# Performance work log

Hardware: AMD Instinct MI355X
Metric: run time of the kernel (lower is better)

## Reference

```python
import jax, jax.numpy as jnp
import numpy as np
import math

NLAT, NLON, LMAX, MMAX = 128, 256, 50, 50
K = 3  # three_nn

# ---- precompute: Clenshaw-Curtis quadrature (torch_harmonics 'equiangular') ----
def _cc_nodes_weights(n):
    Nn = n - 1
    theta = np.pi * np.arange(n) / Nn
    v = np.zeros(n)
    for k in range(1, Nn // 2 + 1):
        b = 1.0 if 2 * k == Nn else 2.0
        v += b * np.cos(2 * k * theta) / (4 * k * k - 1)
    w = (2.0 / Nn) * (1.0 - v)
    w[0] *= 0.5
    w[-1] *= 0.5
    return np.cos(theta), w

# ---- precompute: orthonormal associated Legendre P_l^m(cos theta), csphase ----
def _legpoly(lmax, mmax, cost):
    sint = np.sqrt(np.clip(1.0 - cost ** 2, 0.0, None))
    p = np.zeros((mmax, lmax, cost.shape[0]))
    pmm = np.full(cost.shape[0], np.sqrt(1.0 / (4.0 * np.pi)))
    for m in range(mmax):
        if m > 0:
            pmm = -pmm * np.sqrt((2.0 * m + 1.0) / (2.0 * m)) * sint
        p[m, m] = pmm
        if m + 1 < lmax:
            p[m, m + 1] = np.sqrt(2.0 * m + 3.0) * cost * pmm
        for l in range(m + 2, lmax):
            a = np.sqrt((4.0 * l * l - 1.0) / (l * l - m * m))
            b = np.sqrt(((2.0 * l + 1.0) * (l - 1 + m) * (l - 1 - m)) / ((2.0 * l - 3.0) * (l * l - m * m)))
            p[m, l] = a * cost * p[m, l - 1] - b * p[m, l - 2]
    return p

_cost, _w = _cc_nodes_weights(NLAT)
_PCTW = jnp.asarray((_legpoly(LMAX, MMAX, _cost) * _w[None, None, :]).astype(np.float32))  # (mmax,lmax,nlat)

_gx, _gy = np.meshgrid(np.arange(NLAT), np.arange(-NLAT, NLAT), indexing='ij')
_GRID = jnp.asarray((np.stack([_gx.ravel(), _gy.ravel()], -1) / NLAT * np.pi).astype(np.float32))  # (M,2)

_RECTW = jnp.asarray(np.exp(-(LMAX - np.arange(1, LMAX + 1)) ** 2 / (2.0 * LMAX ** 2)).astype(np.float32))  # (lmax,)


def to_spherical(coords):
    # coords: (B,N,3) -> r:(B,N), sph:(B,N,2) = [arccos(x/r), azimuth in [0,2pi)]
    sq = coords ** 2
    pn = jnp.sqrt(jnp.flip(jnp.cumsum(jnp.flip(sq, -1), -1), -1))  # pn[...,i] = ||coords[...,i:]||
    r = pn[..., 0]
    phi = jnp.arccos(coords[..., :-2] / pn[..., :-2])
    a = jnp.arccos(coords[..., -2] / pn[..., -2])
    phi_final = a + (2.0 * math.pi - 2.0 * a) * (coords[..., -1] < 0)
    return r, jnp.concatenate([phi, phi_final[..., None]], axis=-1)


def interp_to_grid(coords):
    # spherical transform + 3-NN (squared dists) + distance-weighted interpolation onto the lat/lon grid
    r, sph = to_spherical(coords)
    sph = sph.at[..., 1].add(-math.pi)
    # brute-force pairwise squared distances grid(M,2) vs sph(B,N,2): (B,M,N)
    d2 = (jnp.sum(_GRID ** 2, -1)[None, :, None] + jnp.sum(sph ** 2, -1)[:, None, :]
          - 2.0 * jnp.einsum('md,bnd->bmn', _GRID, sph))
    _, idx = jax.lax.top_k(-jax.lax.stop_gradient(d2), K)  # (B,M,K), ascending distance
    sel = jax.vmap(lambda s, i: s[i])(sph, idx)            # (B,M,K,2)
    fsel = jax.vmap(lambda f, i: f[i])(r, idx)             # (B,M,K)
    dk = jnp.sum((_GRID[None, :, None, :] - sel) ** 2, -1)  # recompute selected sq-dists (differentiable)
    w = dk / jnp.sum(dk, -1, keepdims=True)                # weights = dist / sum(dist), as in source
    return jnp.sum(fsel * w, -1).reshape(-1, NLAT, NLON)


def sht_real(x):
    # RealSHT (equiangular, ortho): rfft(norm='forward')*2pi, then Legendre*quadrature einsum; real part only
    xf = jnp.fft.rfft(x, axis=-1)[..., :MMAX] * (2.0 * math.pi / NLON)
    return jnp.einsum('bkm,mlk->blm', jnp.real(xf).astype(jnp.float32), _PCTW)  # (B,lmax,mmax)


def setup_inputs() -> dict:
    key = jax.random.key(0)
    k1, k2 = jax.random.split(key)
    pred = jax.random.normal(k1, (2, 2048, 3), dtype=jnp.float32)
    target = jax.random.normal(k2, (2, 2048, 3), dtype=jnp.float32)
    return {"pred": pred, "target": target}


def reference(pred, target):
    pc = sht_real(interp_to_grid(pred))
    tc = sht_real(interp_to_grid(target))
    return jnp.mean(jnp.sum((pc - tc) ** 2 * _RECTW[None, :, None], axis=(1, 2)))
```

## Files before the change

kernel.cpp:

```cpp
#include <hip/hip_runtime.h>
#include <math.h>

#define PI_D 3.14159265358979323846
#define PIF  3.14159265358979323846f
#define NLAT 128
#define NLON 256
#define LMAX 50
#define MMAX 50
#define NPTS 2048
#define NBT 16
#define NBA 32
#define NBIN (NBT * NBA)
#define WBIN 0.19634954084936207f
#define INVW 5.092958178940651f
#define BIG 1e30f
#define KMASK 0xFFFFF800u

__device__ float2 g_btl[4][NPTS];
__device__ float  g_br[4][NPTS];
__device__ int    g_boff[4][NBIN + 1];
__device__ float  g_pctwT[(size_t)LMAX * NLAT * MMAX];
__device__ float  g_fre[(size_t)4 * NLAT * MMAX];

__device__ __forceinline__ void insert3(float kf, float& k0, float& k1, float& k2) {
    float n1 = __builtin_amdgcn_fmed3f(kf, k0, k1);
    float n2 = __builtin_amdgcn_fmed3f(kf, k1, k2);
    k0 = fminf(kf, k0);
    k1 = n1;
    k2 = n2;
}

__device__ __forceinline__ float mkkey(float gt, float gl, float2 tl, int idx) {
    float dt = gt - tl.x, dl = gl - tl.y;
    float d = fmaf(dt, dt, dl * dl);
    return __uint_as_float((__float_as_uint(d) & KMASK) | (unsigned)idx);
}

__global__ __launch_bounds__(256) void bin_fields(
    const float* __restrict__ pred, const float* __restrict__ tgt) {

    __shared__ int s_cnt[NBIN];
    __shared__ int s_off[NBIN + 1];

    int f = blockIdx.x;
    int t = threadIdx.x;
    const float* src = ((f < 2) ? pred : tgt) + (size_t)(f & 1) * NPTS * 3;

    for (int i = t; i < NBIN; i += 256) s_cnt[i] = 0;
    __syncthreads();

    float pth[8], paz[8], pr[8];
    int pbin[8];
#pragma unroll
    for (int i = 0; i < 8; ++i) {
        int n = t + 256 * i;
        float x = src[3 * n], y = src[3 * n + 1], z = src[3 * n + 2];
        float s1 = z * z;
        float s2 = s1 + y * y;
        float s3 = s2 + x * x;
        float r = sqrtf(s3);
        float rho = sqrtf(s2);
        float th = acosf(x / r);
        float a = acosf(y / rho);
        float az = (z < 0.0f) ? (a + (2.0f * PIF - 2.0f * a)) : a;
        az -= PIF;
        int bt = min(max((int)(th * INVW), 0), NBT - 1);
        int ba = min(max((int)((az + PIF) * INVW), 0), NBA - 1);
        int b = bt * NBA + ba;
        pth[i] = th; paz[i] = az; pr[i] = r; pbin[i] = b;
        atomicAdd(&s_cnt[b], 1);
    }
    __syncthreads();

    if (t == 0) s_off[NBIN] = NPTS;
    if (t < 64) {
        int base = t * 8;
        int loc[8];
        int run = 0;
#pragma unroll
        for (int i = 0; i < 8; ++i) { loc[i] = run; run += s_cnt[base + i]; }
        int x = run;
#pragma unroll
        for (int d = 1; d < 64; d <<= 1) {
            int y = __shfl_up(x, d);
            if (t >= d) x += y;
        }
        int ex = x - run;
#pragma unroll
        for (int i = 0; i < 8; ++i) s_off[base + i] = ex + loc[i];
    }
    __syncthreads();
    for (int i = t; i < NBIN; i += 256) s_cnt[i] = s_off[i];
    for (int i = t; i <= NBIN; i += 256) g_boff[f][i] = s_off[i];
    __syncthreads();
#pragma unroll
    for (int i = 0; i < 8; ++i) {
        int pos = atomicAdd(&s_cnt[pbin[i]], 1);
        g_btl[f][pos] = make_float2(pth[i], paz[i]);
        g_br[f][pos] = pr[i];
    }
}

__global__ __launch_bounds__(256) void query_pctw(float* __restrict__ out) {

    __shared__ int   s_off[NBIN + 1];
    __shared__ float s_row[NLON];
    __shared__ float s_part[256];

    int bid = blockIdx.x;
    int t = threadIdx.x;

    if (bid >= 512) {
        int k = bid - 512;
        int m = t;
        if (k == 0 && m == 0) out[0] = 0.0f;
        if (m >= MMAX) return;

        double thd = PI_D * (double)k / 127.0;
        float cost = (float)cos(thd);
        float sint = (float)sin(thd);

        float c2 = (float)cos(2.0 * thd);
        float two_c2 = 2.0f * c2;
        float cp = 1.0f, cc = c2, v = 0.0f;
        for (int tt = 1; tt <= 63; ++tt) {
            v += 2.0f * cc / (float)(4 * tt * tt - 1);
            float cn = two_c2 * cc - cp;
            cp = cc;
            cc = cn;
        }
        float w = (2.0f / 127.0f) * (1.0f - v);
        if (k == 0 || k == 127) w *= 0.5f;

        float pmm = sqrtf(1.0f / (4.0f * PIF));
        for (int i = 1; i <= m; ++i)
            pmm = -pmm * sqrtf((2.0f * (float)i + 1.0f) / (2.0f * (float)i)) * sint;

        float* o = g_pctwT + (size_t)k * MMAX + m;
        for (int l = 0; l < m; ++l) o[(size_t)l * NLAT * MMAX] = 0.0f;
        o[(size_t)m * NLAT * MMAX] = pmm * w;
        float plm2 = pmm, plm1 = 0.0f;
        if (m + 1 < LMAX) {
            plm1 = sqrtf(2.0f * (float)m + 3.0f) * cost * pmm;
            o[(size_t)(m + 1) * NLAT * MMAX] = plm1 * w;
        }
        for (int l = m + 2; l < LMAX; ++l) {
            float fl = (float)l;
            float denom = fl * fl - (float)(m * m);
            float a = sqrtf((4.0f * fl * fl - 1.0f) / denom);
            float b = sqrtf(((2.0f * fl + 1.0f) * (float)(l - 1 + m) * (float)(l - 1 - m)) /
                            ((2.0f * fl - 3.0f) * denom));
            float p = a * cost * plm1 - b * plm2;
            o[(size_t)l * NLAT * MMAX] = p * w;
            plm2 = plm1;
            plm1 = p;
        }
        return;
    }

    int f = bid >> 7;
    int lat = bid & 127;
    const float2* __restrict__ btl = g_btl[f];
    const float*  __restrict__ br  = g_br[f];

    for (int i = t; i <= NBIN; i += 256) s_off[i] = g_boff[f][i];
    __syncthreads();

    int j = t;
    float gt = (float)((double)lat * PI_D / 128.0);
    float gl = (float)(((double)j - 128.0) * PI_D / 128.0);
    float glp = gl + PIF;
    int bt0 = lat >> 3;
    int ba0 = j >> 3;

    auto scan_seg = [&](int i, int i1, float& q0, float& q1, float& q2) {
        for (; i + 4 <= i1; i += 4) {
            float2 a0 = btl[i];
            float2 a1 = btl[i + 1];
            float2 a2 = btl[i + 2];
            float2 a3 = btl[i + 3];
            insert3(mkkey(gt, gl, a0, i), q0, q1, q2);
            insert3(mkkey(gt, gl, a1, i + 1), q0, q1, q2);
            insert3(mkkey(gt, gl, a2, i + 2), q0, q1, q2);
            insert3(mkkey(gt, gl, a3, i + 3), q0, q1, q2);
        }
        for (; i < i1; ++i)
            insert3(mkkey(gt, gl, btl[i], i), q0, q1, q2);
    };

    float k0 = BIG, k1 = BIG, k2 = BIG;
    {
        int rtl = max(bt0 - 1, 0), rth = min(bt0 + 1, NBT - 1);
        int bal = max(ba0 - 1, 0), bah = min(ba0 + 1, NBA - 1);
        for (int bt = rtl; bt <= rth; ++bt)
            scan_seg(s_off[bt * NBA + bal], s_off[bt * NBA + bah + 1], k0, k1, k2);
    }

    bool done;
    {
        float safe = BIG;
        if (bt0 - 1 > 0)       safe = fminf(safe, gt - (float)(bt0 - 1) * WBIN);
        if (bt0 + 1 < NBT - 1) safe = fminf(safe, (float)(bt0 + 2) * WBIN - gt);
        if (ba0 - 1 > 0)       safe = fminf(safe, glp - (float)(ba0 - 1) * WBIN);
        if (ba0 + 1 < NBA - 1) safe = fminf(safe, (float)(ba0 + 2) * WBIN - glp);
        done = (k2 <= safe * safe);
    }

    for (int R = 2; R <= 31; ++R) {
        if (__all(done)) break;
        if (!done) {
            int btl_ = bt0 - R, bth = bt0 + R;
            int lo = max(btl_, 0), hi = min(bth, NBT - 1);
            int bal = max(ba0 - R, 0), bah = min(ba0 + R, NBA - 1);
            for (int bt = lo; bt <= hi; ++bt) {
                if (bt == btl_ || bt == bth) {
                    scan_seg(s_off[bt * NBA + bal], s_off[bt * NBA + bah + 1], k0, k1, k2);
                } else {
                    if (ba0 - R >= 0) {
                        int b = bt * NBA + ba0 - R;
                        scan_seg(s_off[b], s_off[b + 1], k0, k1, k2);
                    }
                    if (ba0 + R <= NBA - 1) {
                        int b = bt * NBA + ba0 + R;
                        scan_seg(s_off[b], s_off[b + 1], k0, k1, k2);
                    }
                }
            }
            float safe = BIG;
            if (bt0 - R > 0)       safe = fminf(safe, gt - (float)(bt0 - R) * WBIN);
            if (bt0 + R < NBT - 1) safe = fminf(safe, (float)(bt0 + R + 1) * WBIN - gt);
            if (ba0 - R > 0)       safe = fminf(safe, glp - (float)(ba0 - R) * WBIN);
            if (ba0 + R < NBA - 1) safe = fminf(safe, (float)(ba0 + R + 1) * WBIN - glp);
            if (k2 <= safe * safe) done = true;
        }
    }

    {
        int i0 = __float_as_uint(k0) & 0x7FF;
        int i1 = __float_as_uint(k1) & 0x7FF;
        int i2 = __float_as_uint(k2) & 0x7FF;
        float2 p0 = btl[i0];
        float2 p1 = btl[i1];
        float2 p2 = btl[i2];
        float dt0 = gt - p0.x, dl0 = gl - p0.y;
        float dt1 = gt - p1.x, dl1 = gl - p1.y;
        float dt2 = gt - p2.x, dl2 = gl - p2.y;
        float d0 = fmaf(dt0, dt0, dl0 * dl0);
        float d1 = fmaf(dt1, dt1, dl1 * dl1);
        float d2 = fmaf(dt2, dt2, dl2 * dl2);
        float s = d0 + d1 + d2;
        s_row[j] = (d0 * br[i0] + d1 * br[i1] + d2 * br[i2]) / s;
    }
    __syncthreads();

    {
        int q = t >> 6;
        int mm = t & 63;
        if (mm < MMAX) {
            int bs = q * 64;
            const float W0 = 2.0f * PIF / 256.0f;
            float cphi2 = 2.0f * __cosf(W0 * (float)mm);
            float acc = 0.0f;
#pragma unroll
            for (int seg = 0; seg < 4; ++seg) {
                int i0 = bs + seg * 16;
                float c0 = __cosf(W0 * (float)((i0 * mm) & 255));
                float c1 = __cosf(W0 * (float)(((i0 + 1) * mm) & 255));
                acc = fmaf(s_row[i0], c0, acc);
                acc = fmaf(s_row[i0 + 1], c1, acc);
#pragma unroll
                for (int i = 2; i < 16; ++i) {
                    float cn = fmaf(cphi2, c1, -c0);
                    acc = fmaf(s_row[i0 + i], cn, acc);
                    c0 = c1;
                    c1 = cn;
                }
            }
            s_part[q * 64 + mm] = acc;
        }
    }
    __syncthreads();
    if (t < MMAX) {
        int mm = t;
        float v = ((s_part[mm] + s_part[64 + mm]) + (s_part[128 + mm] + s_part[192 + mm])) *
                  (float)(2.0 * PI_D / (double)NLON);
        g_fre[(f * NLAT + lat) * MMAX + mm] = v;
    }
}

__global__ __launch_bounds__(256) void contract_loss(float* __restrict__ out) {
    int b = blockIdx.x / LMAX;
    int l = blockIdx.x % LMAX;
    int mm = threadIdx.x & 63;
    int kq = threadIdx.x >> 6;
    __shared__ float sp[4][64], st_[4][64];
    float pc = 0.0f, tc = 0.0f;
    if (mm < MMAX) {
        const float* pw = g_pctwT + ((size_t)l * NLAT + kq * 32) * MMAX + mm;
        const float* fp = g_fre + ((size_t)b * NLAT + kq * 32) * MMAX + mm;
        const float* ft = g_fre + ((size_t)(2 + b) * NLAT + kq * 32) * MMAX + mm;
#pragma unroll 8
        for (int k = 0; k < 32; ++k) {
            float w = pw[k * MMAX];
            pc += fp[k * MMAX] * w;
            tc += ft[k * MMAX] * w;
        }
    }
    sp[kq][mm] = pc;
    st_[kq][mm] = tc;
    __syncthreads();
    if (threadIdx.x < 64) {
        int m2 = threadIdx.x;
        float pcs = (sp[0][m2] + sp[1][m2]) + (sp[2][m2] + sp[3][m2]);
        float tcs = (st_[0][m2] + st_[1][m2]) + (st_[2][m2] + st_[3][m2]);
        float diff = pcs - tcs;
        double dl_ = (double)(49 - l);
        float rw = (float)exp(-(dl_ * dl_) / 5000.0);
        float contrib = (m2 < MMAX) ? diff * diff * rw * 0.5f : 0.0f;
        for (int off = 32; off > 0; off >>= 1) contrib += __shfl_down(contrib, off);
        if (m2 == 0) atomicAdd(out, contrib);
    }
}

extern "C" void kernel_launch(void* const* d_in, const int* in_sizes, int n_in,
                              void* d_out, int out_size, void* d_ws, size_t ws_size,
                              hipStream_t stream) {
    const float* pred = (const float*)d_in[0];
    const float* tgt = (const float*)d_in[1];
    float* out = (float*)d_out;
    (void)d_ws; (void)ws_size;

    bin_fields<<<4, 256, 0, stream>>>(pred, tgt);
    query_pctw<<<640, 256, 0, stream>>>(out);
    contract_loss<<<2 * LMAX, 256, 0, stream>>>(out);
}
```

Before: 89.42 us.

## Fuse three kernels into one persistent kernel with hierarchical grid barriers

Merges binning, the query/DFT stage and the Legendre contraction into a single 256-block launch that uses two software grid barriers (group counters feeding a root counter) in place of kernel boundaries. Each block now handles two latitude rows instead of one and also computes part of the quadrature-weighted Legendre table. The aim is to remove launch gaps and the tail of the separate precompute blocks. In exchange it relies on all 256 blocks being co-resident for the spin barriers, and it serializes two rows per block, so less parallelism is available during the query phase.

```diff
diff --git a/kernel.cpp b/kernel.cpp
--- a/kernel.cpp
+++ b/kernel.cpp
@@ -15,12 +15,31 @@
 #define INVW 5.092958178940651f
 #define BIG 1e30f
 #define KMASK 0xFFFFF800u
+#define NBLK 256
+#define NGRP 8
 
 __device__ float2 g_btl[4][NPTS];
 __device__ float  g_br[4][NPTS];
 __device__ int    g_boff[4][NBIN + 1];
 __device__ float  g_pctwT[(size_t)LMAX * NLAT * MMAX];
 __device__ float  g_fre[(size_t)4 * NLAT * MMAX];
+
+__device__ int g_grp[2][NGRP][32];
+__device__ int g_root[2][32];
+
+__device__ __forceinline__ void gb_arrive_wait(int phase, int bid, int target) {
+    int g = bid >> 5;
+    int prev = __hip_atomic_fetch_add(&g_grp[phase][g][0], 1,
+                   __ATOMIC_RELAXED, __HIP_MEMORY_SCOPE_AGENT);
+    if ((prev & 31) == 31) {
+        __hip_atomic_fetch_add(&g_root[phase][0], 1,
+                   __ATOMIC_RELAXED, __HIP_MEMORY_SCOPE_AGENT);
+    }
+    while (__hip_atomic_load(&g_root[phase][0],
+                   __ATOMIC_RELAXED, __HIP_MEMORY_SCOPE_AGENT) < target) {
+        __builtin_amdgcn_s_sleep(32);
+    }
+}
 
 __device__ __forceinline__ void insert3(float kf, float& k0, float& k1, float& k2) {
     float n1 = __builtin_amdgcn_fmed3f(kf, k0, k1);
@@ -36,137 +55,9 @@
     return __uint_as_float((__float_as_uint(d) & KMASK) | (unsigned)idx);
 }
 
-__global__ __launch_bounds__(256) void bin_fields(
-    const float* __restrict__ pred, const float* __restrict__ tgt) {
-
-    __shared__ int s_cnt[NBIN];
-    __shared__ int s_off[NBIN + 1];
-
-    int f = blockIdx.x;
-    int t = threadIdx.x;
-    const float* src = ((f < 2) ? pred : tgt) + (size_t)(f & 1) * NPTS * 3;
-
-    for (int i = t; i < NBIN; i += 256) s_cnt[i] = 0;
-    __syncthreads();
-
-    float pth[8], paz[8], pr[8];
-    int pbin[8];
-#pragma unroll
-    for (int i = 0; i < 8; ++i) {
-        int n = t + 256 * i;
-        float x = src[3 * n], y = src[3 * n + 1], z = src[3 * n + 2];
-        float s1 = z * z;
-        float s2 = s1 + y * y;
-        float s3 = s2 + x * x;
-        float r = sqrtf(s3);
-        float rho = sqrtf(s2);
-        float th = acosf(x / r);
-        float a = acosf(y / rho);
-        float az = (z < 0.0f) ? (a + (2.0f * PIF - 2.0f * a)) : a;
-        az -= PIF;
-        int bt = min(max((int)(th * INVW), 0), NBT - 1);
-        int ba = min(max((int)((az + PIF) * INVW), 0), NBA - 1);
-        int b = bt * NBA + ba;
-        pth[i] = th; paz[i] = az; pr[i] = r; pbin[i] = b;
-        atomicAdd(&s_cnt[b], 1);
-    }
-    __syncthreads();
-
-    if (t == 0) s_off[NBIN] = NPTS;
-    if (t < 64) {
-        int base = t * 8;
-        int loc[8];
-        int run = 0;
-#pragma unroll
-        for (int i = 0; i < 8; ++i) { loc[i] = run; run += s_cnt[base + i]; }
-        int x = run;
-#pragma unroll
-        for (int d = 1; d < 64; d <<= 1) {
-            int y = __shfl_up(x, d);
-            if (t >= d) x += y;
-        }
-        int ex = x - run;
-#pragma unroll
-        for (int i = 0; i < 8; ++i) s_off[base + i] = ex + loc[i];
-    }
-    __syncthreads();
-    for (int i = t; i < NBIN; i += 256) s_cnt[i] = s_off[i];
-    for (int i = t; i <= NBIN; i += 256) g_boff[f][i] = s_off[i];
-    __syncthreads();
-#pragma unroll
-    for (int i = 0; i < 8; ++i) {
-        int pos = atomicAdd(&s_cnt[pbin[i]], 1);
-        g_btl[f][pos] = make_float2(pth[i], paz[i]);
-        g_br[f][pos] = pr[i];
-    }
-}
-
-__global__ __launch_bounds__(256) void query_pctw(float* __restrict__ out) {
-
-    __shared__ int   s_off[NBIN + 1];
-    __shared__ float s_row[NLON];
-    __shared__ float s_part[256];
-
-    int bid = blockIdx.x;
-    int t = threadIdx.x;
-
-    if (bid >= 512) {
-        int k = bid - 512;
-        int m = t;
-        if (k == 0 && m == 0) out[0] = 0.0f;
-        if (m >= MMAX) return;
-
-        double thd = PI_D * (double)k / 127.0;
-        float cost = (float)cos(thd);
-        float sint = (float)sin(thd);
-
-        float c2 = (float)cos(2.0 * thd);
-        float two_c2 = 2.0f * c2;
-        float cp = 1.0f, cc = c2, v = 0.0f;
-        for (int tt = 1; tt <= 63; ++tt) {
-            v += 2.0f * cc / (float)(4 * tt * tt - 1);
-            float cn = two_c2 * cc - cp;
-            cp = cc;
-            cc = cn;
-        }
-        float w = (2.0f / 127.0f) * (1.0f - v);
-        if (k == 0 || k == 127) w *= 0.5f;
-
-        float pmm = sqrtf(1.0f / (4.0f * PIF));
-        for (int i = 1; i <= m; ++i)
-            pmm = -pmm * sqrtf((2.0f * (float)i + 1.0f) / (2.0f * (float)i)) * sint;
-
-        float* o = g_pctwT + (size_t)k * MMAX + m;
-        for (int l = 0; l < m; ++l) o[(size_t)l * NLAT * MMAX] = 0.0f;
-        o[(size_t)m * NLAT * MMAX] = pmm * w;
-        float plm2 = pmm, plm1 = 0.0f;
-        if (m + 1 < LMAX) {
-            plm1 = sqrtf(2.0f * (float)m + 3.0f) * cost * pmm;
-            o[(size_t)(m + 1) * NLAT * MMAX] = plm1 * w;
-        }
-        for (int l = m + 2; l < LMAX; ++l) {
-            float fl = (float)l;
-            float denom = fl * fl - (float)(m * m);
-            float a = sqrtf((4.0f * fl * fl - 1.0f) / denom);
-            float b = sqrtf(((2.0f * fl + 1.0f) * (float)(l - 1 + m) * (float)(l - 1 - m)) /
-                            ((2.0f * fl - 3.0f) * denom));
-            float p = a * cost * plm1 - b * plm2;
-            o[(size_t)l * NLAT * MMAX] = p * w;
-            plm2 = plm1;
-            plm1 = p;
-        }
-        return;
-    }
-
-    int f = bid >> 7;
-    int lat = bid & 127;
-    const float2* __restrict__ btl = g_btl[f];
-    const float*  __restrict__ br  = g_br[f];
-
-    for (int i = t; i <= NBIN; i += 256) s_off[i] = g_boff[f][i];
-    __syncthreads();
-
-    int j = t;
+__device__ __forceinline__ float query_row(const float2* __restrict__ btl,
+                                           const float* __restrict__ br,
+                                           const int* s_off, int lat, int j) {
     float gt = (float)((double)lat * PI_D / 128.0);
     float gl = (float)(((double)j - 128.0) * PI_D / 128.0);
     float glp = gl + PIF;
@@ -235,90 +126,243 @@
         }
     }
 
+    int i0 = __float_as_uint(k0) & 0x7FF;
+    int i1 = __float_as_uint(k1) & 0x7FF;
+    int i2 = __float_as_uint(k2) & 0x7FF;
+    float2 p0 = btl[i0];
+    float2 p1 = btl[i1];
+    float2 p2 = btl[i2];
+    float dt0 = gt - p0.x, dl0 = gl - p0.y;
+    float dt1 = gt - p1.x, dl1 = gl - p1.y;
+    float dt2 = gt - p2.x, dl2 = gl - p2.y;
+    float d0 = fmaf(dt0, dt0, dl0 * dl0);
+    float d1 = fmaf(dt1, dt1, dl1 * dl1);
+    float d2 = fmaf(dt2, dt2, dl2 * dl2);
+    float s = d0 + d1 + d2;
+    return (d0 * br[i0] + d1 * br[i1] + d2 * br[i2]) / s;
+}
+
+__device__ __forceinline__ void dft_row(const float* row, float* part, int t) {
+    int q = t >> 6;
+    int mm = t & 63;
+    if (mm < MMAX) {
+        int bs = q * 64;
+        const float W0 = 2.0f * PIF / 256.0f;
+        float cphi2 = 2.0f * __cosf(W0 * (float)mm);
+        float acc = 0.0f;
+#pragma unroll
+        for (int seg = 0; seg < 4; ++seg) {
+            int i0 = bs + seg * 16;
+            float c0 = __cosf(W0 * (float)((i0 * mm) & 255));
+            float c1 = __cosf(W0 * (float)(((i0 + 1) * mm) & 255));
+            acc = fmaf(row[i0], c0, acc);
+            acc = fmaf(row[i0 + 1], c1, acc);
+#pragma unroll
+            for (int i = 2; i < 16; ++i) {
+                float cn = fmaf(cphi2, c1, -c0);
+                acc = fmaf(row[i0 + i], cn, acc);
+                c0 = c1;
+                c1 = cn;
+            }
+        }
+        part[q * 64 + mm] = acc;
+    }
+}
+
+__device__ __forceinline__ void pctw_col(int k, int m) {
+    double thd = PI_D * (double)k / 127.0;
+    float cost = (float)cos(thd);
+    float sint = (float)sin(thd);
+
+    float c2 = (float)cos(2.0 * thd);
+    float two_c2 = 2.0f * c2;
+    float cp = 1.0f, cc = c2, v = 0.0f;
+    for (int tt = 1; tt <= 63; ++tt) {
+        v += 2.0f * cc / (float)(4 * tt * tt - 1);
+        float cn = two_c2 * cc - cp;
+        cp = cc;
+        cc = cn;
+    }
+    float w = (2.0f / 127.0f) * (1.0f - v);
+    if (k == 0 || k == 127) w *= 0.5f;
+
+    float pmm = sqrtf(1.0f / (4.0f * PIF));
+    for (int i = 1; i <= m; ++i)
+        pmm = -pmm * sqrtf((2.0f * (float)i + 1.0f) / (2.0f * (float)i)) * sint;
+
+    float* o = g_pctwT + (size_t)k * MMAX + m;
+    for (int l = 0; l < m; ++l) o[(size_t)l * NLAT * MMAX] = 0.0f;
+    o[(size_t)m * NLAT * MMAX] = pmm * w;
+    float plm2 = pmm, plm1 = 0.0f;
+    if (m + 1 < LMAX) {
+        plm1 = sqrtf(2.0f * (float)m + 3.0f) * cost * pmm;
+        o[(size_t)(m + 1) * NLAT * MMAX] = plm1 * w;
+    }
+    for (int l = m + 2; l < LMAX; ++l) {
+        float fl = (float)l;
+        float denom = fl * fl - (float)(m * m);
+        float a = sqrtf((4.0f * fl * fl - 1.0f) / denom);
+        float b = sqrtf(((2.0f * fl + 1.0f) * (float)(l - 1 + m) * (float)(l - 1 - m)) /
+                        ((2.0f * fl - 3.0f) * denom));
+        float p = a * cost * plm1 - b * plm2;
+        o[(size_t)l * NLAT * MMAX] = p * w;
+        plm2 = plm1;
+        plm1 = p;
+    }
+}
+
+__global__ __launch_bounds__(256) void fused_one(
+    const float* __restrict__ pred, const float* __restrict__ tgt,
+    float* __restrict__ out) {
+
+    __shared__ int   s_cnt[NBIN];
+    __shared__ int   s_off[NBIN + 1];
+    __shared__ float s_row[2][NLON];
+    __shared__ float s_part[256];
+    __shared__ float sp[4][64], st_[4][64];
+
+    int bid = blockIdx.x;
+    int t = threadIdx.x;
+
+    int tgtA = 0, tgtB = 0;
+    if (t == 0) {
+        int e0 = __hip_atomic_load(&g_root[0][0], __ATOMIC_RELAXED, __HIP_MEMORY_SCOPE_AGENT);
+        int e1 = __hip_atomic_load(&g_root[1][0], __ATOMIC_RELAXED, __HIP_MEMORY_SCOPE_AGENT);
+        tgtA = (e0 & ~(NGRP - 1)) + NGRP;
+        tgtB = (e1 & ~(NGRP - 1)) + NGRP;
+    }
+
+    if (bid < 4) {
+        int f = bid;
+        const float* src = ((f < 2) ? pred : tgt) + (size_t)(f & 1) * NPTS * 3;
+        if (bid == 0 && t == 0) out[0] = 0.0f;
+
+        for (int i = t; i < NBIN; i += 256) s_cnt[i] = 0;
+        __syncthreads();
+
+        float pth[8], paz[8], pr[8];
+        int pbin[8];
+#pragma unroll
+        for (int i = 0; i < 8; ++i) {
+            int n = t + 256 * i;
+            float x = src[3 * n], y = src[3 * n + 1], z = src[3 * n + 2];
+            float s1 = z * z;
+            float s2 = s1 + y * y;
+            float s3 = s2 + x * x;
+            float r = sqrtf(s3);
+            float rho = sqrtf(s2);
+            float th = acosf(x / r);
+            float a = acosf(y / rho);
+            float az = (z < 0.0f) ? (a + (2.0f * PIF - 2.0f * a)) : a;
+            az -= PIF;
+            int bt = min(max((int)(th * INVW), 0), NBT - 1);
+            int ba = min(max((int)((az + PIF) * INVW), 0), NBA - 1);
+            int b = bt * NBA + ba;
+            pth[i] = th; paz[i] = az; pr[i] = r; pbin[i] = b;
+            atomicAdd(&s_cnt[b], 1);
+        }
+        __syncthreads();
+
+        if (t == 0) s_off[NBIN] = NPTS;
+        if (t < 64) {
+            int base = t * 8;
+            int loc[8];
+            int run = 0;
+#pragma unroll
+            for (int i = 0; i < 8; ++i) { loc[i] = run; run += s_cnt[base + i]; }
+            int x = run;
+#pragma unroll
+            for (int d = 1; d < 64; d <<= 1) {
+                int y = __shfl_up(x, d);
+                if (t >= d) x += y;
+            }
+            int ex = x - run;
+#pragma unroll
+            for (int i = 0; i < 8; ++i) s_off[base + i] = ex + loc[i];
+        }
+        __syncthreads();
+        for (int i = t; i < NBIN; i += 256) s_cnt[i] = s_off[i];
+        for (int i = t; i <= NBIN; i += 256) g_boff[f][i] = s_off[i];
+        __syncthreads();
+#pragma unroll
+        for (int i = 0; i < 8; ++i) {
+            int pos = atomicAdd(&s_cnt[pbin[i]], 1);
+            g_btl[f][pos] = make_float2(pth[i], paz[i]);
+            g_br[f][pos] = pr[i];
+        }
+    }
+
+    __syncthreads();
+    if (t == 0) { __threadfence(); gb_arrive_wait(0, bid, tgtA); }
+    __syncthreads();
+    __threadfence();
+
     {
-        int i0 = __float_as_uint(k0) & 0x7FF;
-        int i1 = __float_as_uint(k1) & 0x7FF;
-        int i2 = __float_as_uint(k2) & 0x7FF;
-        float2 p0 = btl[i0];
-        float2 p1 = btl[i1];
-        float2 p2 = btl[i2];
-        float dt0 = gt - p0.x, dl0 = gl - p0.y;
-        float dt1 = gt - p1.x, dl1 = gl - p1.y;
-        float dt2 = gt - p2.x, dl2 = gl - p2.y;
-        float d0 = fmaf(dt0, dt0, dl0 * dl0);
-        float d1 = fmaf(dt1, dt1, dl1 * dl1);
-        float d2 = fmaf(dt2, dt2, dl2 * dl2);
-        float s = d0 + d1 + d2;
-        s_row[j] = (d0 * br[i0] + d1 * br[i1] + d2 * br[i2]) / s;
-    }
+        int f = bid >> 6;
+        int lat0 = (bid & 63) * 2;
+        const float2* __restrict__ btl = g_btl[f];
+        const float*  __restrict__ br  = g_br[f];
+
+        for (int i = t; i <= NBIN; i += 256) s_off[i] = g_boff[f][i];
+        __syncthreads();
+
+        s_row[0][t] = query_row(btl, br, s_off, lat0, t);
+        s_row[1][t] = query_row(btl, br, s_off, lat0 + 1, t);
+        __syncthreads();
+
+        dft_row(s_row[0], s_part, t);
+        __syncthreads();
+        if (t < MMAX)
+            g_fre[(f * NLAT + lat0) * MMAX + t] =
+                ((s_part[t] + s_part[64 + t]) + (s_part[128 + t] + s_part[192 + t])) *
+                (float)(2.0 * PI_D / (double)NLON);
+        __syncthreads();
+        dft_row(s_row[1], s_part, t);
+        __syncthreads();
+        if (t < MMAX)
+            g_fre[(f * NLAT + lat0 + 1) * MMAX + t] =
+                ((s_part[t] + s_part[64 + t]) + (s_part[128 + t] + s_part[192 + t])) *
+                (float)(2.0 * PI_D / (double)NLON);
+
+        if (t < 25) pctw_col(bid >> 1, (bid & 1) * 25 + t);
+    }
+
     __syncthreads();
-
-    {
-        int q = t >> 6;
+    if (t == 0) { __threadfence(); gb_arrive_wait(1, bid, tgtB); }
+    __syncthreads();
+    __threadfence();
+
+    if (bid < 2 * LMAX) {
+        int b = bid / LMAX;
+        int l = bid % LMAX;
         int mm = t & 63;
+        int kq = t >> 6;
+        float pc = 0.0f, tc = 0.0f;
         if (mm < MMAX) {
-            int bs = q * 64;
-            const float W0 = 2.0f * PIF / 256.0f;
-            float cphi2 = 2.0f * __cosf(W0 * (float)mm);
-            float acc = 0.0f;
-#pragma unroll
-            for (int seg = 0; seg < 4; ++seg) {
-                int i0 = bs + seg * 16;
-                float c0 = __cosf(W0 * (float)((i0 * mm) & 255));
-                float c1 = __cosf(W0 * (float)(((i0 + 1) * mm) & 255));
-                acc = fmaf(s_row[i0], c0, acc);
-                acc = fmaf(s_row[i0 + 1], c1, acc);
-#pragma unroll
-                for (int i = 2; i < 16; ++i) {
-                    float cn = fmaf(cphi2, c1, -c0);
-                    acc = fmaf(s_row[i0 + i], cn, acc);
-                    c0 = c1;
-                    c1 = cn;
-                }
+            const float* pw = g_pctwT + ((size_t)l * NLAT + kq * 32) * MMAX + mm;
+            const float* fp = g_fre + ((size_t)b * NLAT + kq * 32) * MMAX + mm;
+            const float* ft = g_fre + ((size_t)(2 + b) * NLAT + kq * 32) * MMAX + mm;
+#pragma unroll 8
+            for (int k = 0; k < 32; ++k) {
+                float w = pw[k * MMAX];
+                pc += fp[k * MMAX] * w;
+                tc += ft[k * MMAX] * w;
             }
-            s_part[q * 64 + mm] = acc;
-        }
-    }
-    __syncthreads();
-    if (t < MMAX) {
-        int mm = t;
-        float v = ((s_part[mm] + s_part[64 + mm]) + (s_part[128 + mm] + s_part[192 + mm])) *
-                  (float)(2.0 * PI_D / (double)NLON);
-        g_fre[(f * NLAT + lat) * MMAX + mm] = v;
-    }
-}
-
-__global__ __launch_bounds__(256) void contract_loss(float* __restrict__ out) {
-    int b = blockIdx.x / LMAX;
-    int l = blockIdx.x % LMAX;
-    int mm = threadIdx.x & 63;
-    int kq = threadIdx.x >> 6;
-    __shared__ float sp[4][64], st_[4][64];
-    float pc = 0.0f, tc = 0.0f;
-    if (mm < MMAX) {
-        const float* pw = g_pctwT + ((size_t)l * NLAT + kq * 32) * MMAX + mm;
-        const float* fp = g_fre + ((size_t)b * NLAT + kq * 32) * MMAX + mm;
-        const float* ft = g_fre + ((size_t)(2 + b) * NLAT + kq * 32) * MMAX + mm;
-#pragma unroll 8
-        for (int k = 0; k < 32; ++k) {
-            float w = pw[k * MMAX];
-            pc += fp[k * MMAX] * w;
-            tc += ft[k * MMAX] * w;
-        }
-    }
-    sp[kq][mm] = pc;
-    st_[kq][mm] = tc;
-    __syncthreads();
-    if (threadIdx.x < 64) {
-        int m2 = threadIdx.x;
-        float pcs = (sp[0][m2] + sp[1][m2]) + (sp[2][m2] + sp[3][m2]);
-        float tcs = (st_[0][m2] + st_[1][m2]) + (st_[2][m2] + st_[3][m2]);
-        float diff = pcs - tcs;
-        double dl_ = (double)(49 - l);
-        float rw = (float)exp(-(dl_ * dl_) / 5000.0);
-        float contrib = (m2 < MMAX) ? diff * diff * rw * 0.5f : 0.0f;
-        for (int off = 32; off > 0; off >>= 1) contrib += __shfl_down(contrib, off);
-        if (m2 == 0) atomicAdd(out, contrib);
+        }
+        sp[kq][mm] = pc;
+        st_[kq][mm] = tc;
+        __syncthreads();
+        if (t < 64) {
+            int m2 = t;
+            float pcs = (sp[0][m2] + sp[1][m2]) + (sp[2][m2] + sp[3][m2]);
+            float tcs = (st_[0][m2] + st_[1][m2]) + (st_[2][m2] + st_[3][m2]);
+            float diff = pcs - tcs;
+            double dl_ = (double)(49 - l);
+            float rw = (float)exp(-(dl_ * dl_) / 5000.0);
+            float contrib = (m2 < MMAX) ? diff * diff * rw * 0.5f : 0.0f;
+            for (int off = 32; off > 0; off >>= 1) contrib += __shfl_down(contrib, off);
+            if (m2 == 0) atomicAdd(out, contrib);
+        }
     }
 }
 
@@ -330,7 +374,5 @@
     float* out = (float*)d_out;
     (void)d_ws; (void)ws_size;
 
-    bin_fields<<<4, 256, 0, stream>>>(pred, tgt);
-    query_pctw<<<640, 256, 0, stream>>>(out);
-    contract_loss<<<2 * LMAX, 256, 0, stream>>>(out);
-}
+    fused_one<<<NBLK, 256, 0, stream>>>(pred, tgt, out);
+}
```

After: 133.9 us. 1.5x slower.
